# Performance work log

Measured on AMD Instinct MI355X. Metric: run time of the kernel, lower is better.

Reference implementation:

```python
import jax, jax.numpy as jnp
import numpy as np

N = 100000
E = 800000
D = 128


def setup_inputs() -> dict:
    key = jax.random.key(0)
    k1, k2, k3, k4 = jax.random.split(key, 4)
    x = jax.random.normal(k1, (N, D), dtype=jnp.float32)
    edge_index = jax.random.randint(k2, (2, E), 0, N, dtype=jnp.int64)
    s = 1.0 / np.sqrt(D)
    W1 = jax.random.uniform(k3, (D, D), jnp.float32, -s, s)
    b1 = jnp.zeros((D,), jnp.float32)
    W2 = jax.random.uniform(k4, (D, D), jnp.float32, -s, s)
    b2 = jnp.zeros((D,), jnp.float32)
    return {"x": x, "edge_index": edge_index, "W1": W1, "b1": b1, "W2": W2, "b2": b2}


def _degree(idx, n, dtype):
    return jax.ops.segment_sum(jnp.ones(idx.shape, dtype), idx, num_segments=n)


def _graph_conv(x, row, col, W, b, residual, act):
    n = x.shape[0]
    deg_out = jnp.clip(_degree(row, n, x.dtype), 1.0)          # [N]
    x_src = x * jax.lax.rsqrt(deg_out)[:, None]                # [N, D]
    # scatter-add messages from source (row) into target (col)
    agg = jax.ops.segment_sum(x_src[row], col, num_segments=n)  # [N, D]
    out = agg @ W.T + b
    deg_in = jnp.clip(_degree(col, n, x.dtype), 1.0)
    out = out * jax.lax.rsqrt(deg_in)[:, None]
    if residual:
        out = out + x  # res_fc is Identity (in_dim == out_dim)
    if act:
        out = jax.nn.relu(out)
    return out


def reference(x, edge_index, W1, b1, W2, b2):
    row, col = edge_index[0], edge_index[1]
    # layer 1: relu + residual; layer 2 (last, encoding=False): no act, no residual
    h = _graph_conv(x, row, col, W1, b1, residual=True, act=True)
    h = _graph_conv(h, row, col, W2, b2, residual=False, act=False)
    return h
```

## Files before the change

kernel.cpp:

```cpp
#include <hip/hip_runtime.h>


#define NN 100000
#define EE 800000
#define DD 128
#define NB1 98
#define NTILE (NN / 16)

#define CC 64
#define CH (EE / CC)
#define HALF 50000
#define HWORDS 12500
#define NWORDS 25000

typedef __attribute__((ext_vector_type(8))) short short8;
typedef __attribute__((ext_vector_type(4))) float floatx4;

__device__ inline float bf2f(unsigned int u16) {
    union { unsigned int i; float f; } c;
    c.i = u16 << 16;
    return c.f;
}
__device__ inline ushort f2bf(float f) {
    union { float f; unsigned int i; } c;
    c.f = f;
    unsigned int u = c.i;
    return (ushort)((u + 0x7fffu + ((u >> 16) & 1u)) >> 16);
}

__global__ __launch_bounds__(512) void count_kernel(const int* __restrict__ row,
                                                    const int* __restrict__ col,
                                                    unsigned int* __restrict__ partial_out,
                                                    unsigned int* __restrict__ partial_in,
                                                    unsigned char* __restrict__ off_u8) {
    __shared__ unsigned int h[HWORDS];
    for (int i = threadIdx.x; i < HWORDS; i += 512) h[i] = 0;
    __syncthreads();

    const int kind = blockIdx.x >> 7;
    const int r = (blockIdx.x >> 6) & 1;
    const int c = blockIdx.x & 63;
    const int* __restrict__ idx = kind ? row : col;
    const int base = c * CH;
    const int lo = r * HALF;

    for (int t = threadIdx.x; t < CH; t += 512) {
        const int e = base + t;
        const unsigned int d = (unsigned int)(idx[e] - lo);
        if (d < (unsigned int)HALF) {
            const int sh = 8 * (d & 3);
            unsigned int old = atomicAdd(&h[d >> 2], 1u << sh);
            if (kind == 0) off_u8[e] = (unsigned char)((old >> sh) & 0xffu);
        }
    }
    __syncthreads();

    unsigned int* dst = (kind ? partial_out : partial_in) + c * NWORDS + r * HWORDS;
    for (int i = threadIdx.x; i < HWORDS; i += 512) dst[i] = h[i];
}

__global__ __launch_bounds__(256) void node_kernel(const unsigned int* __restrict__ partial_out,
                                                   const unsigned int* __restrict__ partial_in,
                                                   int* __restrict__ cnt_total,
                                                   unsigned int* __restrict__ xoff,
                                                   float* __restrict__ dinv_out,
                                                   float* __restrict__ dinv_in) {
    const int w = blockIdx.x * 256 + threadIdx.x;
    if (w >= NWORDS) return;
    unsigned int prefix = 0;
    unsigned int tot_out = 0;
#pragma unroll
    for (int c = 0; c < CC; ++c) {
        unsigned int v = partial_in[c * NWORDS + w];
        xoff[c * NWORDS + w] = prefix;
        prefix += v;
        tot_out += partial_out[c * NWORDS + w];
    }
    int4 ct;
    float4 fi, fo;
#pragma unroll
    for (int j = 0; j < 4; ++j) {
        int din  = (int)((prefix  >> (8 * j)) & 0xffu);
        int dout = (int)((tot_out >> (8 * j)) & 0xffu);
        ((int*)&ct)[j]   = din;
        ((float*)&fi)[j] = rsqrtf((float)max(din, 1));
        ((float*)&fo)[j] = rsqrtf((float)max(dout, 1));
    }
    ((int4*)cnt_total)[w] = ct;
    ((float4*)dinv_in)[w] = fi;
    ((float4*)dinv_out)[w] = fo;
}

__global__ __launch_bounds__(256) void scan1_kernel(const int* __restrict__ cnt,
                                                    int* __restrict__ excl,
                                                    int* __restrict__ bsums) {
    __shared__ int tmp[256];
    const int t = threadIdx.x;
    const int base = blockIdx.x * 1024 + t * 4;
    int a[4];
#pragma unroll
    for (int q = 0; q < 4; ++q) a[q] = (base + q < NN) ? cnt[base + q] : 0;
    int s = a[0] + a[1] + a[2] + a[3];
    tmp[t] = s;
    __syncthreads();
    for (int off = 1; off < 256; off <<= 1) {
        int v = 0;
        if (t >= off) v = tmp[t - off];
        __syncthreads();
        tmp[t] += v;
        __syncthreads();
    }
    int excl_s = tmp[t] - s;
    if (t == 255) bsums[blockIdx.x] = tmp[t];
    int run = excl_s;
#pragma unroll
    for (int q = 0; q < 4; ++q) {
        if (base + q < NN) excl[base + q] = run;
        run += a[q];
    }
}

__global__ __launch_bounds__(256) void scan2_kernel(int* __restrict__ bsums, int nb) {
    __shared__ int tmp[256];
    const int t = threadIdx.x;
    int s = (t < nb) ? bsums[t] : 0;
    tmp[t] = s;
    __syncthreads();
    for (int off = 1; off < 256; off <<= 1) {
        int v = 0;
        if (t >= off) v = tmp[t - off];
        __syncthreads();
        tmp[t] += v;
        __syncthreads();
    }
    if (t < nb) bsums[t] = tmp[t] - s;
}

__global__ __launch_bounds__(256) void scan3_kernel(const int* __restrict__ excl,
                                                    const int* __restrict__ bsums,
                                                    int* __restrict__ row_start) {
    int i = blockIdx.x * 256 + threadIdx.x;
    if (i < NN) row_start[i] = excl[i] + bsums[i >> 10];
}

__global__ __launch_bounds__(256) void fill_kernel(const int* __restrict__ row,
                                                   const int* __restrict__ col,
                                                   const int* __restrict__ row_start,
                                                   const unsigned char* __restrict__ xoff_u8,
                                                   const unsigned char* __restrict__ off_u8,
                                                   int* __restrict__ srcs) {
    int e = blockIdx.x * 256 + threadIdx.x;
    if (e < EE) {
        const int cl = col[e];
        const int c = e / CH;
        const int pos = row_start[cl] + (int)xoff_u8[(size_t)c * NN + cl] + (int)off_u8[e];
        srcs[pos] = row[e];
    }
}

__global__ __launch_bounds__(256) void prescale_kernel(const float* __restrict__ x,
                                                       const float* __restrict__ dinv_out,
                                                       ushort* __restrict__ xb) {
    int idx = blockIdx.x * 256 + threadIdx.x;
    if (idx >= NN * 32) return;
    int n = idx >> 5;
    float s = dinv_out[n];
    float4 v = ((const float4*)x)[idx];
    ushort4 o;
    o.x = f2bf(v.x * s);
    o.y = f2bf(v.y * s);
    o.z = f2bf(v.z * s);
    o.w = f2bf(v.w * s);
    ((ushort4*)xb)[idx] = o;
}

__global__ __launch_bounds__(256) void wconv_kernel(const float* __restrict__ W1,
                                                    const float* __restrict__ W2,
                                                    ushort* __restrict__ wb1,
                                                    ushort* __restrict__ wb2) {
    int i = blockIdx.x * 256 + threadIdx.x;
    if (i >= 8192) return;
    const float* W = (i < 4096) ? W1 : W2;
    ushort* wb = (i < 4096) ? wb1 : wb2;
    int j = i & 4095;
    float4 v = ((const float4*)W)[j];
    ushort4 o;
    o.x = f2bf(v.x); o.y = f2bf(v.y); o.z = f2bf(v.z); o.w = f2bf(v.w);
    ((ushort4*)wb)[j] = o;
}

__global__ __launch_bounds__(256) void gather_kernel(const ushort* __restrict__ src,
                                                     const int* __restrict__ row_start,
                                                     const int* __restrict__ srcs,
                                                     ushort* __restrict__ agg) {
    const int node = blockIdx.x * 16 + (threadIdx.x >> 4);
    const int lane = threadIdx.x & 15;
    if (node >= NN) return;
    int p = row_start[node];
    const int end = (node + 1 < NN) ? row_start[node + 1] : EE;
    float a0 = 0.f, a1 = 0.f, a2 = 0.f, a3 = 0.f;
    float a4 = 0.f, a5 = 0.f, a6 = 0.f, a7 = 0.f;

#define ACCUM(V)                                     \
    do {                                             \
        a0 += bf2f((V).x & 0xffffu);                 \
        a1 += bf2f((V).x >> 16);                     \
        a2 += bf2f((V).y & 0xffffu);                 \
        a3 += bf2f((V).y >> 16);                     \
        a4 += bf2f((V).z & 0xffffu);                 \
        a5 += bf2f((V).z >> 16);                     \
        a6 += bf2f((V).w & 0xffffu);                 \
        a7 += bf2f((V).w >> 16);                     \
    } while (0)

    for (; p + 3 < end; p += 4) {
        int s0 = srcs[p];
        int s1 = srcs[p + 1];
        int s2 = srcs[p + 2];
        int s3 = srcs[p + 3];
        uint4 v0 = ((const uint4*)(src + (size_t)s0 * DD))[lane];
        uint4 v1 = ((const uint4*)(src + (size_t)s1 * DD))[lane];
        uint4 v2 = ((const uint4*)(src + (size_t)s2 * DD))[lane];
        uint4 v3 = ((const uint4*)(src + (size_t)s3 * DD))[lane];
        ACCUM(v0); ACCUM(v1); ACCUM(v2); ACCUM(v3);
    }
    for (; p < end; ++p) {
        int s0 = srcs[p];
        uint4 v0 = ((const uint4*)(src + (size_t)s0 * DD))[lane];
        ACCUM(v0);
    }
#undef ACCUM

    uint4 o;
    o.x = (unsigned int)f2bf(a0) | ((unsigned int)f2bf(a1) << 16);
    o.y = (unsigned int)f2bf(a2) | ((unsigned int)f2bf(a3) << 16);
    o.z = (unsigned int)f2bf(a4) | ((unsigned int)f2bf(a5) << 16);
    o.w = (unsigned int)f2bf(a6) | ((unsigned int)f2bf(a7) << 16);
    ((uint4*)(agg + (size_t)node * DD))[lane] = o;
}

template <bool L1>
__global__ __launch_bounds__(256) void gemm_ep(const ushort* __restrict__ agg,
                                               const ushort* __restrict__ wb,
                                               const float* __restrict__ bias,
                                               const float* __restrict__ dinv_in,
                                               const float* __restrict__ dinv_out,
                                               const float* __restrict__ x,
                                               ushort* __restrict__ hs,
                                               float* __restrict__ out) {
    __shared__ ushort Ws[128 * 136];
    {
        int j = threadIdx.x >> 1;
        int k0 = (threadIdx.x & 1) * 64;
        const uint4* wp = (const uint4*)(wb + (size_t)j * DD + k0);
        uint4* dst = (uint4*)(Ws + j * 136 + k0);
#pragma unroll
        for (int q = 0; q < 8; ++q) dst[q] = wp[q];
    }
    __syncthreads();

    const int wave = threadIdx.x >> 6;
    const int lane = threadIdx.x & 63;
    const int tile = blockIdx.x * 4 + wave;
    if (tile >= NTILE) return;
    const int mi = lane & 15;
    const int quad = lane >> 4;
    const int m0 = tile * 16;

    floatx4 acc[8];
#pragma unroll
    for (int t = 0; t < 8; ++t) acc[t] = (floatx4){0.f, 0.f, 0.f, 0.f};

    const ushort* ap = agg + (size_t)(m0 + mi) * DD + quad * 8;
#pragma unroll
    for (int s = 0; s < 4; ++s) {
        short8 a = *(const short8*)(ap + s * 32);
#pragma unroll
        for (int t = 0; t < 8; ++t) {
            short8 b = *(const short8*)(Ws + (t * 16 + mi) * 136 + s * 32 + quad * 8);
            acc[t] = __builtin_amdgcn_mfma_f32_16x16x32_bf16(a, b, acc[t], 0, 0, 0);
        }
    }

    float dv[4], dov[4];
#pragma unroll
    for (int i = 0; i < 4; ++i) {
        int r = m0 + quad * 4 + i;
        dv[i] = dinv_in[r];
        if (L1) dov[i] = dinv_out[r];
    }
#pragma unroll
    for (int t = 0; t < 8; ++t) {
        int c = t * 16 + mi;
        float bv = bias[c];
#pragma unroll
        for (int i = 0; i < 4; ++i) {
            int r = m0 + quad * 4 + i;
            float o = (acc[t][i] + bv) * dv[i];
            if (L1) {
                o += x[(size_t)r * DD + c];
                o = fmaxf(o, 0.f);
                hs[(size_t)r * DD + c] = f2bf(o * dov[i]);
            } else {
                out[(size_t)r * DD + c] = o;
            }
        }
    }
}

extern "C" void kernel_launch(void* const* d_in, const int* in_sizes, int n_in,
                              void* d_out, int out_size, void* d_ws, size_t ws_size,
                              hipStream_t stream) {
    const float* x  = (const float*)d_in[0];
    const int*   ei = (const int*)d_in[1];
    const float* W1 = (const float*)d_in[2];
    const float* b1 = (const float*)d_in[3];
    const float* W2 = (const float*)d_in[4];
    const float* b2 = (const float*)d_in[5];
    float* out = (float*)d_out;

    const int* row = ei;
    const int* col = ei + EE;

    ushort* agg     = (ushort*)d_ws;
    ushort* xb      = agg + (size_t)NN * DD;
    float* dinv_out = (float*)(xb + (size_t)NN * DD);
    float* dinv_in  = dinv_out + NN;
    int*   cnt      = (int*)(dinv_in + NN);
    int*   excl     = cnt + NN;
    int*   row_st   = excl + NN;
    int*   srcs     = row_st + NN;
    int*   bsums    = srcs + EE;
    ushort* wb1     = (ushort*)(bsums + 256);
    ushort* wb2     = wb1 + DD * DD;

    unsigned char* off_u8      = (unsigned char*)agg;
    unsigned int*  partial_in  = (unsigned int*)(off_u8 + EE);
    unsigned int*  partial_out = partial_in + CC * NWORDS;
    unsigned int*  xoff        = partial_out + CC * NWORDS;

    wconv_kernel<<<32, 256, 0, stream>>>(W1, W2, wb1, wb2);
    count_kernel<<<256, 512, 0, stream>>>(row, col, partial_out, partial_in, off_u8);
    node_kernel<<<(NWORDS + 255) / 256, 256, 0, stream>>>(partial_out, partial_in, cnt, xoff,
                                                          dinv_out, dinv_in);
    scan1_kernel<<<NB1, 256, 0, stream>>>(cnt, excl, bsums);
    scan2_kernel<<<1, 256, 0, stream>>>(bsums, NB1);
    scan3_kernel<<<(NN + 255) / 256, 256, 0, stream>>>(excl, bsums, row_st);
    fill_kernel<<<(EE + 255) / 256, 256, 0, stream>>>(row, col, row_st,
                                                      (const unsigned char*)xoff, off_u8, srcs);

    prescale_kernel<<<(NN * 32 + 255) / 256, 256, 0, stream>>>(x, dinv_out, xb);
    gather_kernel<<<(NN + 15) / 16, 256, 0, stream>>>(xb, row_st, srcs, agg);
    gemm_ep<true><<<(NTILE + 3) / 4, 256, 0, stream>>>(agg, wb1, b1, dinv_in, dinv_out, x,
                                                       xb, nullptr);

    gather_kernel<<<(NN + 15) / 16, 256, 0, stream>>>(xb, row_st, srcs, agg);
    gemm_ep<false><<<(NTILE + 3) / 4, 256, 0, stream>>>(agg, wb2, b2, dinv_in, nullptr, nullptr,
                                                        nullptr, out);
}
```

Measured before the change: 267.5 us.

## Use full wave per node in gather and two tiles per wave in GEMM

The gather kernel now assigns a whole 64-lane wave to each destination node, with four 16-lane slots processing different edges concurrently and reducing via cross-lane shuffles. This aims to raise memory-level parallelism for the random row gathers, at the cost of idle lanes on low-degree nodes and shuffle overhead. The GEMM epilogue kernel computes two 16-row tiles per wave so each LDS weight fragment feeds two MFMAs, halving the LDS weight reads per output row.

Result: slower. 290.0 us (+8.4%).

```diff
diff --git a/kernel.cpp b/kernel.cpp
--- a/kernel.cpp
+++ b/kernel.cpp
@@ -193,9 +193,10 @@
                                                      const int* __restrict__ row_start,
                                                      const int* __restrict__ srcs,
                                                      ushort* __restrict__ agg) {
-    const int node = blockIdx.x * 16 + (threadIdx.x >> 4);
-    const int lane = threadIdx.x & 15;
-    if (node >= NN) return;
+    const int node = blockIdx.x * 4 + (threadIdx.x >> 6);
+    const int lane = threadIdx.x & 63;
+    const int slot = lane >> 4;
+    const int lane16 = lane & 15;
     int p = row_start[node];
     const int end = (node + 1 < NN) ? row_start[node + 1] : EE;
     float a0 = 0.f, a1 = 0.f, a2 = 0.f, a3 = 0.f;
@@ -213,30 +214,43 @@
         a7 += bf2f((V).w >> 16);                     \
     } while (0)
 
-    for (; p + 3 < end; p += 4) {
-        int s0 = srcs[p];
-        int s1 = srcs[p + 1];
-        int s2 = srcs[p + 2];
-        int s3 = srcs[p + 3];
-        uint4 v0 = ((const uint4*)(src + (size_t)s0 * DD))[lane];
-        uint4 v1 = ((const uint4*)(src + (size_t)s1 * DD))[lane];
-        uint4 v2 = ((const uint4*)(src + (size_t)s2 * DD))[lane];
-        uint4 v3 = ((const uint4*)(src + (size_t)s3 * DD))[lane];
-        ACCUM(v0); ACCUM(v1); ACCUM(v2); ACCUM(v3);
-    }
-    for (; p < end; ++p) {
-        int s0 = srcs[p];
-        uint4 v0 = ((const uint4*)(src + (size_t)s0 * DD))[lane];
-        ACCUM(v0);
+    for (; p + 8 <= end; p += 8) {
+        int sA = srcs[p + slot];
+        int sB = srcs[p + 4 + slot];
+        uint4 vA = ((const uint4*)(src + (size_t)sA * DD))[lane16];
+        uint4 vB = ((const uint4*)(src + (size_t)sB * DD))[lane16];
+        ACCUM(vA); ACCUM(vB);
+    }
+    if (p + 4 <= end) {
+        int sA = srcs[p + slot];
+        uint4 vA = ((const uint4*)(src + (size_t)sA * DD))[lane16];
+        ACCUM(vA);
+        p += 4;
+    }
+    if (p + slot < end) {
+        int sA = srcs[p + slot];
+        uint4 vA = ((const uint4*)(src + (size_t)sA * DD))[lane16];
+        ACCUM(vA);
     }
 #undef ACCUM
 
-    uint4 o;
-    o.x = (unsigned int)f2bf(a0) | ((unsigned int)f2bf(a1) << 16);
-    o.y = (unsigned int)f2bf(a2) | ((unsigned int)f2bf(a3) << 16);
-    o.z = (unsigned int)f2bf(a4) | ((unsigned int)f2bf(a5) << 16);
-    o.w = (unsigned int)f2bf(a6) | ((unsigned int)f2bf(a7) << 16);
-    ((uint4*)(agg + (size_t)node * DD))[lane] = o;
+    a0 += __shfl_xor(a0, 16, 64); a0 += __shfl_xor(a0, 32, 64);
+    a1 += __shfl_xor(a1, 16, 64); a1 += __shfl_xor(a1, 32, 64);
+    a2 += __shfl_xor(a2, 16, 64); a2 += __shfl_xor(a2, 32, 64);
+    a3 += __shfl_xor(a3, 16, 64); a3 += __shfl_xor(a3, 32, 64);
+    a4 += __shfl_xor(a4, 16, 64); a4 += __shfl_xor(a4, 32, 64);
+    a5 += __shfl_xor(a5, 16, 64); a5 += __shfl_xor(a5, 32, 64);
+    a6 += __shfl_xor(a6, 16, 64); a6 += __shfl_xor(a6, 32, 64);
+    a7 += __shfl_xor(a7, 16, 64); a7 += __shfl_xor(a7, 32, 64);
+
+    if (slot == 0) {
+        uint4 o;
+        o.x = (unsigned int)f2bf(a0) | ((unsigned int)f2bf(a1) << 16);
+        o.y = (unsigned int)f2bf(a2) | ((unsigned int)f2bf(a3) << 16);
+        o.z = (unsigned int)f2bf(a4) | ((unsigned int)f2bf(a5) << 16);
+        o.w = (unsigned int)f2bf(a6) | ((unsigned int)f2bf(a7) << 16);
+        ((uint4*)(agg + (size_t)node * DD))[lane16] = o;
+    }
 }
 
 template <bool L1>
@@ -261,48 +275,58 @@
 
     const int wave = threadIdx.x >> 6;
     const int lane = threadIdx.x & 63;
-    const int tile = blockIdx.x * 4 + wave;
-    if (tile >= NTILE) return;
+    const int tbase = blockIdx.x * 8 + wave * 2;
+    if (tbase >= NTILE) return;
     const int mi = lane & 15;
     const int quad = lane >> 4;
-    const int m0 = tile * 16;
-
-    floatx4 acc[8];
-#pragma unroll
-    for (int t = 0; t < 8; ++t) acc[t] = (floatx4){0.f, 0.f, 0.f, 0.f};
-
-    const ushort* ap = agg + (size_t)(m0 + mi) * DD + quad * 8;
+
+    floatx4 acc[2][8];
+#pragma unroll
+    for (int u = 0; u < 2; ++u)
+#pragma unroll
+        for (int t = 0; t < 8; ++t) acc[u][t] = (floatx4){0.f, 0.f, 0.f, 0.f};
+
+    const ushort* ap0 = agg + (size_t)(tbase * 16 + mi) * DD + quad * 8;
+    const ushort* ap1 = ap0 + (size_t)16 * DD;
 #pragma unroll
     for (int s = 0; s < 4; ++s) {
-        short8 a = *(const short8*)(ap + s * 32);
+        short8 A0 = *(const short8*)(ap0 + s * 32);
+        short8 A1 = *(const short8*)(ap1 + s * 32);
 #pragma unroll
         for (int t = 0; t < 8; ++t) {
             short8 b = *(const short8*)(Ws + (t * 16 + mi) * 136 + s * 32 + quad * 8);
-            acc[t] = __builtin_amdgcn_mfma_f32_16x16x32_bf16(a, b, acc[t], 0, 0, 0);
+            acc[0][t] = __builtin_amdgcn_mfma_f32_16x16x32_bf16(A0, b, acc[0][t], 0, 0, 0);
+            acc[1][t] = __builtin_amdgcn_mfma_f32_16x16x32_bf16(A1, b, acc[1][t], 0, 0, 0);
         }
     }
 
-    float dv[4], dov[4];
-#pragma unroll
-    for (int i = 0; i < 4; ++i) {
-        int r = m0 + quad * 4 + i;
-        dv[i] = dinv_in[r];
-        if (L1) dov[i] = dinv_out[r];
-    }
-#pragma unroll
-    for (int t = 0; t < 8; ++t) {
-        int c = t * 16 + mi;
-        float bv = bias[c];
+#pragma unroll
+    for (int u = 0; u < 2; ++u) {
+        const int tile = tbase + u;
+        if (tile >= NTILE) break;
+        const int m0 = tile * 16;
+        float dv[4], dov[4];
 #pragma unroll
         for (int i = 0; i < 4; ++i) {
             int r = m0 + quad * 4 + i;
-            float o = (acc[t][i] + bv) * dv[i];
-            if (L1) {
-                o += x[(size_t)r * DD + c];
-                o = fmaxf(o, 0.f);
-                hs[(size_t)r * DD + c] = f2bf(o * dov[i]);
-            } else {
-                out[(size_t)r * DD + c] = o;
+            dv[i] = dinv_in[r];
+            if (L1) dov[i] = dinv_out[r];
+        }
+#pragma unroll
+        for (int t = 0; t < 8; ++t) {
+            int c = t * 16 + mi;
+            float bv = bias[c];
+#pragma unroll
+            for (int i = 0; i < 4; ++i) {
+                int r = m0 + quad * 4 + i;
+                float o = (acc[u][t][i] + bv) * dv[i];
+                if (L1) {
+                    o += x[(size_t)r * DD + c];
+                    o = fmaxf(o, 0.f);
+                    hs[(size_t)r * DD + c] = f2bf(o * dov[i]);
+                } else {
+                    out[(size_t)r * DD + c] = o;
+                }
             }
         }
     }
@@ -350,11 +374,11 @@
                                                       (const unsigned char*)xoff, off_u8, srcs);
 
     prescale_kernel<<<(NN * 32 + 255) / 256, 256, 0, stream>>>(x, dinv_out, xb);
-    gather_kernel<<<(NN + 15) / 16, 256, 0, stream>>>(xb, row_st, srcs, agg);
-    gemm_ep<true><<<(NTILE + 3) / 4, 256, 0, stream>>>(agg, wb1, b1, dinv_in, dinv_out, x,
+    gather_kernel<<<NN / 4, 256, 0, stream>>>(xb, row_st, srcs, agg);
+    gemm_ep<true><<<(NTILE + 7) / 8, 256, 0, stream>>>(agg, wb1, b1, dinv_in, dinv_out, x,
                                                        xb, nullptr);
 
-    gather_kernel<<<(NN + 15) / 16, 256, 0, stream>>>(xb, row_st, srcs, agg);
-    gemm_ep<false><<<(NTILE + 3) / 4, 256, 0, stream>>>(agg, wb2, b2, dinv_in, nullptr, nullptr,
+    gather_kernel<<<NN / 4, 256, 0, stream>>>(xb, row_st, srcs, agg);
+    gemm_ep<false><<<(NTILE + 7) / 8, 256, 0, stream>>>(agg, wb2, b2, dinv_in, nullptr, nullptr,
                                                         nullptr, out);
 }
```
